# Performance work log

Hardware: AMD Instinct MI355X
Metric: run time of the kernel (lower is better)

The kernel has to match this reference:

```python
import jax, jax.numpy as jnp
import numpy as np

B, D, L, H = 512, 512, 32, 300  # batch, input_dim, latent_dim, hidden_dim


def setup_inputs() -> dict:
    key = jax.random.key(0)
    ks = jax.random.split(key, 16)
    s = lambda k, *sh: jax.random.normal(k, sh, dtype=jnp.float32) * 0.05
    return {
        "x": jax.random.normal(ks[0], (B, D), dtype=jnp.float32),
        "eps": jax.random.normal(ks[1], (B, L), dtype=jnp.float32),
        "W": jax.random.normal(ks[2], (D, L), dtype=jnp.float32),  # mask (get_generator_mask -> W)
        "qz_w1": s(ks[3], D, H), "qz_b1": s(ks[4], H),
        "qz_w2": s(ks[5], H, H), "qz_b2": s(ks[6], H),
        "zm_w": s(ks[7], H, L), "zm_b": s(ks[8], L),
        "zl_w": s(ks[9], H, L), "zl_b": s(ks[10], L),
        "gen_w1": s(ks[11], L, H),               # no bias (bias=False)
        "gen_w2": s(ks[12], H, H), "gen_b2": s(ks[13], H),
        "col_w": s(ks[14], D, H), "col_b": s(ks[15], D),  # stacked column_means Linears
    }


def reference(x, eps, W, qz_w1, qz_b1, qz_w2, qz_b2, zm_w, zm_b, zl_w, zl_b,
              gen_w1, gen_w2, gen_b2, col_w, col_b):
    # encode
    h = jax.nn.relu(x @ qz_w1 + qz_b1)
    h = jax.nn.relu(h @ qz_w2 + qz_b2)
    z_mean = h @ zm_w + zm_b
    z_log_var = h @ zl_w + zl_b
    # reparameterize (eps supplied as input)
    z = z_mean + eps * jnp.exp(0.5 * z_log_var)
    # decode: per-column masked generator MLP, batched over columns j
    masked = W[:, None, :] * z[None, :, :]                 # [D, B, L]
    g = jax.nn.relu(jnp.einsum('jbl,lh->jbh', masked, gen_w1))
    g = jax.nn.relu(jnp.einsum('jbh,hk->jbk', g, gen_w2) + gen_b2)
    x_rec = jnp.einsum('jbh,jh->jb', g, col_w) + col_b[:, None]  # [D, B]
    x_mean = x_rec.T                                       # [B, D]
    return (x_mean, z, z_mean, z_log_var)
```

## Files before the change

kernel.cpp:

```cpp
#include <hip/hip_runtime.h>

#define B_ 512
#define D_ 512
#define L_ 32
#define H_ 300
#define NT 19
#define NS 10
#define G1S 308
#define HS 312

typedef unsigned short ushort_t;
typedef __bf16 bf16x8 __attribute__((ext_vector_type(8)));
typedef float f32x4 __attribute__((ext_vector_type(4)));

union B8 { ushort_t u[8]; uint4 q; bf16x8 v; uint2 d[2]; __bf16 b[8]; };

__device__ __forceinline__ void split8(const float* fv, B8& hi, B8& lo) {
    #pragma unroll
    for (int i = 0; i < 8; ++i) {
        __bf16 h = (__bf16)fv[i];
        hi.b[i] = h;
        lo.b[i] = (__bf16)(fv[i] - (float)h);
    }
}

__global__ __launch_bounds__(64) void prep_kernel(
        const float* __restrict__ gw1, const float* __restrict__ gw2,
        const float* __restrict__ qw1, const float* __restrict__ qw2,
        const float* __restrict__ zmw, const float* __restrict__ zlw,
        ushort_t* __restrict__ gw1f, ushort_t* __restrict__ gw2f,
        ushort_t* __restrict__ w1hi, ushort_t* __restrict__ w1lo,
        ushort_t* __restrict__ w2hi, ushort_t* __restrict__ w2lo,
        ushort_t* __restrict__ w3hi, ushort_t* __restrict__ w3lo) {
    int blk = blockIdx.x;
    int l = threadIdx.x, grp = l >> 4, li = l & 15;
    if (blk < 209) {
        const float* src; int K, nt, s; ushort_t* dst;
        if (blk < 19) { nt = blk; s = 0; src = gw1; K = 32; dst = gw1f + (nt * 64 + l) * 8; }
        else { int i = blk - 19; nt = i / 10; s = i % 10; src = gw2; K = 300;
               dst = gw2f + ((nt * 10 + s) * 64 + l) * 8; }
        int n = nt * 16 + li;
        B8 V;
        #pragma unroll
        for (int i = 0; i < 8; ++i) {
            int k = 32 * s + 8 * grp + i;
            V.b[i] = (__bf16)((k < K && n < H_) ? src[k * H_ + n] : 0.f);
        }
        *reinterpret_cast<uint4*>(dst) = V.q;
    } else {
        const float* src = nullptr; int K, N, nt, s, stacked = 0;
        ushort_t *dh, *dl;
        if (blk < 513)      { int i = blk - 209; nt = i / 16; s = i % 16; src = qw1; K = 512; N = 300;
                              dh = w1hi + ((nt * 16 + s) * 64 + l) * 8; dl = w1lo + ((nt * 16 + s) * 64 + l) * 8; }
        else if (blk < 703) { int i = blk - 513; nt = i / 10; s = i % 10; src = qw2; K = 300; N = 300;
                              dh = w2hi + ((nt * 10 + s) * 64 + l) * 8; dl = w2lo + ((nt * 10 + s) * 64 + l) * 8; }
        else                { int i = blk - 703; nt = i / 10; s = i % 10; K = 300; N = 64; stacked = 1;
                              dh = w3hi + ((nt * 10 + s) * 64 + l) * 8; dl = w3lo + ((nt * 10 + s) * 64 + l) * 8; }
        int n = nt * 16 + li;
        float fv[8];
        #pragma unroll
        for (int i = 0; i < 8; ++i) {
            int k = 32 * s + 8 * grp + i;
            float v = 0.f;
            if (k < K && n < N) {
                if (!stacked) v = src[k * N + n];
                else          v = (n < 32) ? zmw[k * 32 + n] : zlw[k * 32 + (n - 32)];
            }
            fv[i] = v;
        }
        B8 Vh, Vl;
        split8(fv, Vh, Vl);
        *reinterpret_cast<uint4*>(dh) = Vh.q;
        *reinterpret_cast<uint4*>(dl) = Vl.q;
    }
}

__global__ __launch_bounds__(256) void fused_encoder(
        const float* __restrict__ x,
        const ushort_t* __restrict__ w1hi, const ushort_t* __restrict__ w1lo,
        const ushort_t* __restrict__ w2hi, const ushort_t* __restrict__ w2lo,
        const ushort_t* __restrict__ w3hi, const ushort_t* __restrict__ w3lo,
        const float* __restrict__ b1, const float* __restrict__ b2,
        const float* __restrict__ zmb, const float* __restrict__ zlb,
        const float* __restrict__ eps, float* __restrict__ out,
        float* __restrict__ zb) {
    __shared__ __align__(16) ushort_t hs1_hi[16 * HS + 16], hs1_lo[16 * HS + 16];
    __shared__ __align__(16) ushort_t hs2_hi[16 * HS + 16], hs2_lo[16 * HS + 16];
    __shared__ float zs2[64][17];

    const int tid = threadIdx.x;
    const int w = tid >> 6, lane = tid & 63;
    const int grp = lane >> 4, li = lane & 15;
    const int r0 = blockIdx.x * 16;
    const int nlocal = (w == 3) ? 4 : 5;

    for (int idx = tid; idx < 16 * 8 + 16; idx += 256) {
        int off = (idx < 128) ? ((idx >> 3) * HS + 304 + (idx & 7)) : (16 * HS + (idx - 128));
        hs1_hi[off] = 0; hs1_lo[off] = 0; hs2_hi[off] = 0; hs2_lo[off] = 0;
    }
    __syncthreads();

    {
        f32x4 acc[5];
        #pragma unroll
        for (int i = 0; i < 5; ++i) acc[i] = {0.f, 0.f, 0.f, 0.f};
        for (int s = 0; s < 16; ++s) {
            const float* ap = x + (size_t)(r0 + li) * 512 + 32 * s + 8 * grp;
            float4 f0 = *reinterpret_cast<const float4*>(ap);
            float4 f1 = *reinterpret_cast<const float4*>(ap + 4);
            float fv[8] = {f0.x, f0.y, f0.z, f0.w, f1.x, f1.y, f1.z, f1.w};
            B8 Bh, Bl;
            split8(fv, Bh, Bl);
            #pragma unroll
            for (int ntl = 0; ntl < 5; ++ntl) {
                if (ntl < nlocal) {
                    int nt = w * 5 + ntl;
                    bf16x8 Ah = *reinterpret_cast<const bf16x8*>(
                        w1hi + ((size_t)(nt * 16 + s) * 64 + lane) * 8);
                    bf16x8 Al = *reinterpret_cast<const bf16x8*>(
                        w1lo + ((size_t)(nt * 16 + s) * 64 + lane) * 8);
                    acc[ntl] = __builtin_amdgcn_mfma_f32_16x16x32_bf16(Ah, Bh.v, acc[ntl], 0, 0, 0);
                    acc[ntl] = __builtin_amdgcn_mfma_f32_16x16x32_bf16(Al, Bh.v, acc[ntl], 0, 0, 0);
                    acc[ntl] = __builtin_amdgcn_mfma_f32_16x16x32_bf16(Ah, Bl.v, acc[ntl], 0, 0, 0);
                }
            }
        }
        #pragma unroll
        for (int ntl = 0; ntl < 5; ++ntl) {
            if (ntl < nlocal) {
                int nt = w * 5 + ntl;
                B8 Ph, Pl;
                #pragma unroll
                for (int r = 0; r < 4; ++r) {
                    int h = nt * 16 + 4 * grp + r;
                    float v = (h < H_) ? fmaxf(acc[ntl][r] + b1[h], 0.f) : 0.f;
                    __bf16 hb = (__bf16)v;
                    Ph.b[r] = hb;
                    Pl.b[r] = (__bf16)(v - (float)hb);
                }
                int off = li * HS + nt * 16 + 4 * grp;
                *reinterpret_cast<uint2*>(&hs1_hi[off]) = Ph.d[0];
                *reinterpret_cast<uint2*>(&hs1_lo[off]) = Pl.d[0];
            }
        }
    }
    __syncthreads();

    {
        f32x4 acc[5];
        #pragma unroll
        for (int i = 0; i < 5; ++i) acc[i] = {0.f, 0.f, 0.f, 0.f};
        for (int s = 0; s < NS; ++s) {
            int off = li * HS + 32 * s + 8 * grp;
            B8 Bh, Bl;
            Bh.q = *reinterpret_cast<const uint4*>(&hs1_hi[off]);
            Bl.q = *reinterpret_cast<const uint4*>(&hs1_lo[off]);
            #pragma unroll
            for (int ntl = 0; ntl < 5; ++ntl) {
                if (ntl < nlocal) {
                    int nt = w * 5 + ntl;
                    bf16x8 Ah = *reinterpret_cast<const bf16x8*>(
                        w2hi + ((size_t)(nt * 10 + s) * 64 + lane) * 8);
                    bf16x8 Al = *reinterpret_cast<const bf16x8*>(
                        w2lo + ((size_t)(nt * 10 + s) * 64 + lane) * 8);
                    acc[ntl] = __builtin_amdgcn_mfma_f32_16x16x32_bf16(Ah, Bh.v, acc[ntl], 0, 0, 0);
                    acc[ntl] = __builtin_amdgcn_mfma_f32_16x16x32_bf16(Al, Bh.v, acc[ntl], 0, 0, 0);
                    acc[ntl] = __builtin_amdgcn_mfma_f32_16x16x32_bf16(Ah, Bl.v, acc[ntl], 0, 0, 0);
                }
            }
        }
        #pragma unroll
        for (int ntl = 0; ntl < 5; ++ntl) {
            if (ntl < nlocal) {
                int nt = w * 5 + ntl;
                B8 Ph, Pl;
                #pragma unroll
                for (int r = 0; r < 4; ++r) {
                    int h = nt * 16 + 4 * grp + r;
                    float v = (h < H_) ? fmaxf(acc[ntl][r] + b2[h], 0.f) : 0.f;
                    __bf16 hb = (__bf16)v;
                    Ph.b[r] = hb;
                    Pl.b[r] = (__bf16)(v - (float)hb);
                }
                int off = li * HS + nt * 16 + 4 * grp;
                *reinterpret_cast<uint2*>(&hs2_hi[off]) = Ph.d[0];
                *reinterpret_cast<uint2*>(&hs2_lo[off]) = Pl.d[0];
            }
        }
    }
    __syncthreads();

    {
        f32x4 acc = {0.f, 0.f, 0.f, 0.f};
        for (int s = 0; s < NS; ++s) {
            int off = li * HS + 32 * s + 8 * grp;
            B8 Bh, Bl;
            Bh.q = *reinterpret_cast<const uint4*>(&hs2_hi[off]);
            Bl.q = *reinterpret_cast<const uint4*>(&hs2_lo[off]);
            bf16x8 Ah = *reinterpret_cast<const bf16x8*>(
                w3hi + ((size_t)(w * 10 + s) * 64 + lane) * 8);
            bf16x8 Al = *reinterpret_cast<const bf16x8*>(
                w3lo + ((size_t)(w * 10 + s) * 64 + lane) * 8);
            acc = __builtin_amdgcn_mfma_f32_16x16x32_bf16(Ah, Bh.v, acc, 0, 0, 0);
            acc = __builtin_amdgcn_mfma_f32_16x16x32_bf16(Al, Bh.v, acc, 0, 0, 0);
            acc = __builtin_amdgcn_mfma_f32_16x16x32_bf16(Ah, Bl.v, acc, 0, 0, 0);
        }
        #pragma unroll
        for (int r = 0; r < 4; ++r) zs2[w * 16 + 4 * grp + r][li] = acc[r];
    }
    __syncthreads();

    for (int idx = tid; idx < 512; idx += 256) {
        int m = idx >> 5, l2 = idx & 31;
        int row = r0 + m;
        float zm = zs2[l2][m] + zmb[l2];
        float zl = zs2[32 + l2][m] + zlb[l2];
        float zv = zm + eps[row * 32 + l2] * expf(0.5f * zl);
        out[B_ * D_ + row * 32 + l2] = zv;
        out[B_ * D_ + B_ * L_ + row * 32 + l2] = zm;
        out[B_ * D_ + 2 * B_ * L_ + row * 32 + l2] = zl;
        zb[row * 32 + l2] = zv;
    }
}

__global__ __launch_bounds__(256, 3) void decode_kernel(
        const float* __restrict__ z, const float* __restrict__ Wmask,
        const ushort_t* __restrict__ gw1f, const ushort_t* __restrict__ gw2f,
        const float* __restrict__ gb2, const float* __restrict__ colw,
        const float* __restrict__ colb, float* __restrict__ xmean) {
    __shared__ __align__(16) ushort_t g1s[64 * G1S + 16];
    __shared__ float xpart[4][64];

    const int j    = blockIdx.y;
    const int b0   = blockIdx.x * 64;
    const int tid  = threadIdx.x;
    const int w    = tid >> 6;
    const int lane = tid & 63;
    const int grp  = lane >> 4, li = lane & 15;
    const int nlocal = (w == 3) ? 4 : 5;

    B8 bm[4];
    {
        const float* wp = Wmask + (size_t)j * L_ + 8 * grp;
        float4 w0 = *reinterpret_cast<const float4*>(wp);
        float4 w1 = *reinterpret_cast<const float4*>(wp + 4);
        float wv[8] = {w0.x, w0.y, w0.z, w0.w, w1.x, w1.y, w1.z, w1.w};
        #pragma unroll
        for (int mt = 0; mt < 4; ++mt) {
            const float* zp = z + (size_t)(b0 + mt * 16 + li) * L_ + 8 * grp;
            float4 z0 = *reinterpret_cast<const float4*>(zp);
            float4 z1 = *reinterpret_cast<const float4*>(zp + 4);
            float zv[8] = {z0.x, z0.y, z0.z, z0.w, z1.x, z1.y, z1.z, z1.w};
            #pragma unroll
            for (int i = 0; i < 8; ++i) bm[mt].b[i] = (__bf16)(wv[i] * zv[i]);
        }
        for (int idx = tid; idx < 272; idx += 256) {
            if (idx < 256) g1s[(idx >> 2) * G1S + 304 + (idx & 3)] = 0;
            else           g1s[64 * G1S + (idx - 256)] = 0;
        }
    }
    __syncthreads();

    {
        ushort_t* st = &g1s[li * G1S + 4 * grp];
        #pragma unroll
        for (int ntl = 0; ntl < 5; ++ntl) {
            if (ntl < nlocal) {
                int nt = w * 5 + ntl;
                bf16x8 ga = *reinterpret_cast<const bf16x8*>(gw1f + (nt * 64 + lane) * 8);
                #pragma unroll
                for (int mt = 0; mt < 4; ++mt) {
                    f32x4 c = {0.f, 0.f, 0.f, 0.f};
                    c = __builtin_amdgcn_mfma_f32_16x16x32_bf16(ga, bm[mt].v, c, 0, 0, 0);
                    B8 P;
                    #pragma unroll
                    for (int r = 0; r < 4; ++r) P.b[r] = (__bf16)fmaxf(c[r], 0.f);
                    *reinterpret_cast<uint2*>(st + mt * 16 * G1S + nt * 16) = P.d[0];
                }
            }
        }
    }
    __syncthreads();

    float partial[4][4] = {};
    {
        f32x4 acc[4][5];
        #pragma unroll
        for (int mt = 0; mt < 4; ++mt)
            #pragma unroll
            for (int n = 0; n < 5; ++n) acc[mt][n] = {0.f, 0.f, 0.f, 0.f};

        const size_t lane8 = (size_t)lane * 8;
        for (int s = 0; s < NS; ++s) {
            B8 af[4];
            #pragma unroll
            for (int mt = 0; mt < 4; ++mt) {
                const ushort_t* p = &g1s[(mt * 16 + li) * G1S + 32 * s + 8 * grp];
                af[mt].d[0] = *reinterpret_cast<const uint2*>(p);
                af[mt].d[1] = *reinterpret_cast<const uint2*>(p + 4);
            }
            #pragma unroll
            for (int ntl = 0; ntl < 5; ++ntl) {
                if (ntl < nlocal) {
                    bf16x8 bfr = *reinterpret_cast<const bf16x8*>(
                        gw2f + (size_t)((w * 5 + ntl) * NS + s) * 512 + lane8);
                    #pragma unroll
                    for (int mt = 0; mt < 4; ++mt)
                        acc[mt][ntl] = __builtin_amdgcn_mfma_f32_16x16x32_bf16(
                            af[mt].v, bfr, acc[mt][ntl], 0, 0, 0);
                }
            }
        }

        #pragma unroll
        for (int ntl = 0; ntl < 5; ++ntl) {
            if (ntl < nlocal) {
                int h = (w * 5 + ntl) * 16 + li;
                float bias = 0.f, fac = 0.f;
                if (h < H_) { bias = gb2[h]; fac = colw[j * H_ + h]; }
                #pragma unroll
                for (int mt = 0; mt < 4; ++mt)
                    #pragma unroll
                    for (int r = 0; r < 4; ++r)
                        partial[mt][r] += fmaxf(acc[mt][ntl][r] + bias, 0.f) * fac;
            }
        }
    }
    #pragma unroll
    for (int mt = 0; mt < 4; ++mt)
        #pragma unroll
        for (int r = 0; r < 4; ++r) {
            float v = partial[mt][r];
            v += __shfl_xor(v, 1);
            v += __shfl_xor(v, 2);
            v += __shfl_xor(v, 4);
            v += __shfl_xor(v, 8);
            if (li == 0) xpart[w][mt * 16 + 4 * grp + r] = v;
        }
    __syncthreads();

    if (tid < 64) {
        float v = colb[j];
        #pragma unroll
        for (int ww = 0; ww < 4; ++ww) v += xpart[ww][tid];
        xmean[(size_t)(b0 + tid) * D_ + j] = v;
    }
}

extern "C" void kernel_launch(void* const* d_in, const int* in_sizes, int n_in,
                              void* d_out, int out_size, void* d_ws, size_t ws_size,
                              hipStream_t stream) {
    const float* x     = (const float*)d_in[0];
    const float* eps   = (const float*)d_in[1];
    const float* Wm    = (const float*)d_in[2];
    const float* qz_w1 = (const float*)d_in[3];
    const float* qz_b1 = (const float*)d_in[4];
    const float* qz_w2 = (const float*)d_in[5];
    const float* qz_b2 = (const float*)d_in[6];
    const float* zm_w  = (const float*)d_in[7];
    const float* zm_b  = (const float*)d_in[8];
    const float* zl_w  = (const float*)d_in[9];
    const float* zl_b  = (const float*)d_in[10];
    const float* gw1   = (const float*)d_in[11];
    const float* gw2   = (const float*)d_in[12];
    const float* gb2   = (const float*)d_in[13];
    const float* colw  = (const float*)d_in[14];
    const float* colb  = (const float*)d_in[15];
    float* out = (float*)d_out;
    char* ws = (char*)d_ws;

    ushort_t* gw1f = (ushort_t*)(ws + 0);
    ushort_t* gw2f = (ushort_t*)(ws + 19456);
    ushort_t* w1hi = (ushort_t*)(ws + 214016);
    ushort_t* w1lo = (ushort_t*)(ws + 525312);
    ushort_t* w2hi = (ushort_t*)(ws + 836608);
    ushort_t* w2lo = (ushort_t*)(ws + 1031168);
    ushort_t* w3hi = (ushort_t*)(ws + 1225728);
    ushort_t* w3lo = (ushort_t*)(ws + 1266688);
    float*    zb   = (float*)(ws + 1307648);

    prep_kernel<<<743, 64, 0, stream>>>(gw1, gw2, qz_w1, qz_w2, zm_w, zl_w,
                                        gw1f, gw2f, w1hi, w1lo, w2hi, w2lo, w3hi, w3lo);
    fused_encoder<<<32, 256, 0, stream>>>(x, w1hi, w1lo, w2hi, w2lo, w3hi, w3lo,
                                          qz_b1, qz_b2, zm_b, zl_b, eps, out, zb);
    decode_kernel<<<dim3(8, 512), 256, 0, stream>>>(zb, Wm, gw1f, gw2f, gb2, colw, colb, out);
}
```

Measured before the change: 115.5 us.

## Widen encoder to 8 waves and double-buffer decoder weight fragments

The encoder now launches 512 threads per block. Its 19 hidden tiles are split as 3,3,3,2,2,2,2,2 across 8 waves, so each wave holds fewer accumulators, and the final latent projection runs on the first 4 waves only. The decoder's second GEMM loop is unrolled by two, with register double-buffered loads of the gw2f B fragments so global loads overlap the MFMA work. This adds register pressure in the decoder, and it makes one redundant prefetch on the last iteration.

```diff
diff --git a/kernel.cpp b/kernel.cpp
--- a/kernel.cpp
+++ b/kernel.cpp
@@ -75,7 +75,7 @@
     }
 }
 
-__global__ __launch_bounds__(256) void fused_encoder(
+__global__ __launch_bounds__(512) void fused_encoder(
         const float* __restrict__ x,
         const ushort_t* __restrict__ w1hi, const ushort_t* __restrict__ w1lo,
         const ushort_t* __restrict__ w2hi, const ushort_t* __restrict__ w2lo,
@@ -92,18 +92,19 @@
     const int w = tid >> 6, lane = tid & 63;
     const int grp = lane >> 4, li = lane & 15;
     const int r0 = blockIdx.x * 16;
-    const int nlocal = (w == 3) ? 4 : 5;
-
-    for (int idx = tid; idx < 16 * 8 + 16; idx += 256) {
+    const int nlocal = (w < 3) ? 3 : 2;
+    const int nbeg   = (w < 3) ? w * 3 : 9 + (w - 3) * 2;
+
+    for (int idx = tid; idx < 16 * 8 + 16; idx += 512) {
         int off = (idx < 128) ? ((idx >> 3) * HS + 304 + (idx & 7)) : (16 * HS + (idx - 128));
         hs1_hi[off] = 0; hs1_lo[off] = 0; hs2_hi[off] = 0; hs2_lo[off] = 0;
     }
     __syncthreads();
 
     {
-        f32x4 acc[5];
-        #pragma unroll
-        for (int i = 0; i < 5; ++i) acc[i] = {0.f, 0.f, 0.f, 0.f};
+        f32x4 acc[3];
+        #pragma unroll
+        for (int i = 0; i < 3; ++i) acc[i] = {0.f, 0.f, 0.f, 0.f};
         for (int s = 0; s < 16; ++s) {
             const float* ap = x + (size_t)(r0 + li) * 512 + 32 * s + 8 * grp;
             float4 f0 = *reinterpret_cast<const float4*>(ap);
@@ -112,9 +113,9 @@
             B8 Bh, Bl;
             split8(fv, Bh, Bl);
             #pragma unroll
-            for (int ntl = 0; ntl < 5; ++ntl) {
+            for (int ntl = 0; ntl < 3; ++ntl) {
                 if (ntl < nlocal) {
-                    int nt = w * 5 + ntl;
+                    int nt = nbeg + ntl;
                     bf16x8 Ah = *reinterpret_cast<const bf16x8*>(
                         w1hi + ((size_t)(nt * 16 + s) * 64 + lane) * 8);
                     bf16x8 Al = *reinterpret_cast<const bf16x8*>(
@@ -126,9 +127,9 @@
             }
         }
         #pragma unroll
-        for (int ntl = 0; ntl < 5; ++ntl) {
+        for (int ntl = 0; ntl < 3; ++ntl) {
             if (ntl < nlocal) {
-                int nt = w * 5 + ntl;
+                int nt = nbeg + ntl;
                 B8 Ph, Pl;
                 #pragma unroll
                 for (int r = 0; r < 4; ++r) {
@@ -147,18 +148,18 @@
     __syncthreads();
 
     {
-        f32x4 acc[5];
-        #pragma unroll
-        for (int i = 0; i < 5; ++i) acc[i] = {0.f, 0.f, 0.f, 0.f};
+        f32x4 acc[3];
+        #pragma unroll
+        for (int i = 0; i < 3; ++i) acc[i] = {0.f, 0.f, 0.f, 0.f};
         for (int s = 0; s < NS; ++s) {
             int off = li * HS + 32 * s + 8 * grp;
             B8 Bh, Bl;
             Bh.q = *reinterpret_cast<const uint4*>(&hs1_hi[off]);
             Bl.q = *reinterpret_cast<const uint4*>(&hs1_lo[off]);
             #pragma unroll
-            for (int ntl = 0; ntl < 5; ++ntl) {
+            for (int ntl = 0; ntl < 3; ++ntl) {
                 if (ntl < nlocal) {
-                    int nt = w * 5 + ntl;
+                    int nt = nbeg + ntl;
                     bf16x8 Ah = *reinterpret_cast<const bf16x8*>(
                         w2hi + ((size_t)(nt * 10 + s) * 64 + lane) * 8);
                     bf16x8 Al = *reinterpret_cast<const bf16x8*>(
@@ -170,9 +171,9 @@
             }
         }
         #pragma unroll
-        for (int ntl = 0; ntl < 5; ++ntl) {
+        for (int ntl = 0; ntl < 3; ++ntl) {
             if (ntl < nlocal) {
-                int nt = w * 5 + ntl;
+                int nt = nbeg + ntl;
                 B8 Ph, Pl;
                 #pragma unroll
                 for (int r = 0; r < 4; ++r) {
@@ -190,7 +191,7 @@
     }
     __syncthreads();
 
-    {
+    if (w < 4) {
         f32x4 acc = {0.f, 0.f, 0.f, 0.f};
         for (int s = 0; s < NS; ++s) {
             int off = li * HS + 32 * s + 8 * grp;
@@ -210,8 +211,8 @@
     }
     __syncthreads();
 
-    for (int idx = tid; idx < 512; idx += 256) {
-        int m = idx >> 5, l2 = idx & 31;
+    {
+        int m = tid >> 5, l2 = tid & 31;
         int row = r0 + m;
         float zm = zs2[l2][m] + zmb[l2];
         float zl = zs2[32 + l2][m] + zlb[l2];
@@ -238,6 +239,14 @@
     const int lane = tid & 63;
     const int grp  = lane >> 4, li = lane & 15;
     const int nlocal = (w == 3) ? 4 : 5;
+    const size_t lane8 = (size_t)lane * 8;
+
+    bf16x8 bc[5], bn[5];
+    #pragma unroll
+    for (int ntl = 0; ntl < 5; ++ntl)
+        if (ntl < nlocal)
+            bc[ntl] = *reinterpret_cast<const bf16x8*>(
+                gw2f + (size_t)((w * 5 + ntl) * NS) * 512 + lane8);
 
     B8 bm[4];
     {
@@ -290,25 +299,49 @@
             #pragma unroll
             for (int n = 0; n < 5; ++n) acc[mt][n] = {0.f, 0.f, 0.f, 0.f};
 
-        const size_t lane8 = (size_t)lane * 8;
-        for (int s = 0; s < NS; ++s) {
-            B8 af[4];
-            #pragma unroll
-            for (int mt = 0; mt < 4; ++mt) {
-                const ushort_t* p = &g1s[(mt * 16 + li) * G1S + 32 * s + 8 * grp];
-                af[mt].d[0] = *reinterpret_cast<const uint2*>(p);
-                af[mt].d[1] = *reinterpret_cast<const uint2*>(p + 4);
-            }
-            #pragma unroll
-            for (int ntl = 0; ntl < 5; ++ntl) {
-                if (ntl < nlocal) {
-                    bf16x8 bfr = *reinterpret_cast<const bf16x8*>(
-                        gw2f + (size_t)((w * 5 + ntl) * NS + s) * 512 + lane8);
-                    #pragma unroll
-                    for (int mt = 0; mt < 4; ++mt)
-                        acc[mt][ntl] = __builtin_amdgcn_mfma_f32_16x16x32_bf16(
-                            af[mt].v, bfr, acc[mt][ntl], 0, 0, 0);
-                }
+        for (int s = 0; s < NS; s += 2) {
+            #pragma unroll
+            for (int ntl = 0; ntl < 5; ++ntl)
+                if (ntl < nlocal)
+                    bn[ntl] = *reinterpret_cast<const bf16x8*>(
+                        gw2f + (size_t)((w * 5 + ntl) * NS + s + 1) * 512 + lane8);
+            {
+                B8 af[4];
+                #pragma unroll
+                for (int mt = 0; mt < 4; ++mt) {
+                    const ushort_t* p = &g1s[(mt * 16 + li) * G1S + 32 * s + 8 * grp];
+                    af[mt].d[0] = *reinterpret_cast<const uint2*>(p);
+                    af[mt].d[1] = *reinterpret_cast<const uint2*>(p + 4);
+                }
+                #pragma unroll
+                for (int ntl = 0; ntl < 5; ++ntl)
+                    if (ntl < nlocal)
+                        #pragma unroll
+                        for (int mt = 0; mt < 4; ++mt)
+                            acc[mt][ntl] = __builtin_amdgcn_mfma_f32_16x16x32_bf16(
+                                af[mt].v, bc[ntl], acc[mt][ntl], 0, 0, 0);
+            }
+            int s2 = (s + 2 < NS) ? (s + 2) : 0;
+            #pragma unroll
+            for (int ntl = 0; ntl < 5; ++ntl)
+                if (ntl < nlocal)
+                    bc[ntl] = *reinterpret_cast<const bf16x8*>(
+                        gw2f + (size_t)((w * 5 + ntl) * NS + s2) * 512 + lane8);
+            {
+                B8 af[4];
+                #pragma unroll
+                for (int mt = 0; mt < 4; ++mt) {
+                    const ushort_t* p = &g1s[(mt * 16 + li) * G1S + 32 * (s + 1) + 8 * grp];
+                    af[mt].d[0] = *reinterpret_cast<const uint2*>(p);
+                    af[mt].d[1] = *reinterpret_cast<const uint2*>(p + 4);
+                }
+                #pragma unroll
+                for (int ntl = 0; ntl < 5; ++ntl)
+                    if (ntl < nlocal)
+                        #pragma unroll
+                        for (int mt = 0; mt < 4; ++mt)
+                            acc[mt][ntl] = __builtin_amdgcn_mfma_f32_16x16x32_bf16(
+                                af[mt].v, bn[ntl], acc[mt][ntl], 0, 0, 0);
             }
         }
 
@@ -381,7 +414,7 @@
 
     prep_kernel<<<743, 64, 0, stream>>>(gw1, gw2, qz_w1, qz_w2, zm_w, zl_w,
                                         gw1f, gw2f, w1hi, w1lo, w2hi, w2lo, w3hi, w3lo);
-    fused_encoder<<<32, 256, 0, stream>>>(x, w1hi, w1lo, w2hi, w2lo, w3hi, w3lo,
+    fused_encoder<<<32, 512, 0, stream>>>(x, w1hi, w1lo, w2hi, w2lo, w3hi, w3lo,
                                           qz_b1, qz_b2, zm_b, zl_b, eps, out, zb);
     decode_kernel<<<dim3(8, 512), 256, 0, stream>>>(zb, Wm, gw1f, gw2f, gb2, colw, colb, out);
 }
```

Result: slower. 181.2 us (+56.8%).
